# Kernel tuning notes

Measured on AMD Instinct MI355X. Metric: run time of the kernel, lower is better.

The kernel has to match this reference:

```python
import jax, jax.numpy as jnp
import numpy as np
import math

B, S, DM, H, F = 2, 2048, 1024, 16, 192  # F = head_dim init arg; per-head dim = F // 3
DH = F // 3
MAX_BIAS = 8.0


def _get_slopes(n):
    # faithful to ALiBiBias._get_slopes
    def pow2(n):
        start = 2.0 ** (-(2.0 ** (-(math.log2(n) - 3))))
        return [start * start ** i for i in range(n)]
    if math.log2(n).is_integer():
        return pow2(n)
    cp2 = 2 ** math.floor(math.log2(n))
    return pow2(cp2) + _get_slopes(2 * cp2)[0::2][: n - cp2]


def _rope_sin_cos(seq_len, dim):
    inv_freq = 1.0 / (10000.0 ** (jnp.arange(0, dim, 2, dtype=jnp.float32) / dim))
    freqs = jnp.outer(jnp.arange(seq_len, dtype=jnp.float32), inv_freq)  # [S, dim/2]
    # repeat(sin[:,None,:],2,axis=1).reshape(S,-1) == concat([sin,sin],-1)
    sin = jnp.concatenate([jnp.sin(freqs), jnp.sin(freqs)], axis=-1)  # [S, dim]
    cos = jnp.concatenate([jnp.cos(freqs), jnp.cos(freqs)], axis=-1)
    return sin, cos


def _rotate_half(x):
    x1, x2 = jnp.split(x, 2, axis=-1)
    return jnp.concatenate([-x2, x1], axis=-1)


def setup_inputs() -> dict:
    key = jax.random.key(0)
    kx, kq, ko = jax.random.split(key, 3)
    x = jax.random.normal(kx, (B, S, DM), dtype=jnp.float32)
    w_qkv = jax.random.normal(kq, (DM, H, F), dtype=jnp.float32) * (1.0 / math.sqrt(DM))
    b_qkv = jnp.zeros((H, F), dtype=jnp.float32)
    w_out = jax.random.normal(ko, (H, DH, DM), dtype=jnp.float32) * (1.0 / math.sqrt(H * DH))
    b_out = jnp.zeros((DM,), dtype=jnp.float32)
    return {"x": x, "w_qkv": w_qkv, "b_qkv": b_qkv, "w_out": w_out, "b_out": b_out}


def reference(x, w_qkv, b_qkv, w_out, b_out):
    b, s, dm = x.shape
    h, f = w_qkv.shape[1], w_qkv.shape[2]
    dh = f // 3
    # fused QKV projection: [B,S,H,F], then 3-way split on the feature axis
    qkv = jnp.einsum('bsd,dhf->bshf', x, w_qkv) + b_qkv
    q, k, v = jnp.split(qkv, 3, axis=-1)  # each [B,S,H,DH]
    # RoPE (rotate_half convention), broadcast over heads
    sin, cos = _rope_sin_cos(s, dh)
    sin, cos = sin[:, None, :], cos[:, None, :]  # [S,1,DH]
    q = q * cos + _rotate_half(q) * sin
    k = k * cos + _rotate_half(k) * sin
    # [B,H,S,DH]
    q = q.transpose(0, 2, 1, 3)
    k = k.transpose(0, 2, 1, 3)
    v = v.transpose(0, 2, 1, 3)
    # scores scaled by sqrt(head_dim init arg), as in the original non-flash path
    scores = jnp.einsum('bhqd,bhkd->bhqk', q, k) / jnp.sqrt(jnp.float32(f))
    # ALiBi bias
    slopes = jnp.asarray(_get_slopes(h), dtype=jnp.float32)  # [H]
    pos = jnp.arange(s, dtype=jnp.float32)
    rel = pos[None, :] - pos[:, None]  # j - i
    rel = jnp.where(rel > 0, 0.0, rel)
    alibi = rel[None, :, :] * slopes[:, None, None] * MAX_BIAS  # [H,S,S]
    scores = scores + alibi[None]  # [B,H,S,S]
    # causal mask
    causal = jnp.tril(jnp.ones((s, s), dtype=jnp.float32))
    scores = jnp.where(causal == 0, -1e9, scores)
    weights = jax.nn.softmax(scores, axis=-1)
    attn = jnp.einsum('bhqk,bhkd->bhqd', weights, v).transpose(0, 2, 1, 3)  # [B,S,H,DH]
    return jnp.einsum('bshd,hdm->bsm', attn, w_out) + b_out
```

## Files before the change

### kernel.cpp

```cpp
#include <hip/hip_runtime.h>
#include <math.h>

static constexpr int B_  = 2;
static constexpr int S_  = 2048;
static constexpr int H_  = 16;
static constexpr int DH_ = 64;
static constexpr float QSCALE2_ = 0.104117589f;
static constexpr float C8L2_    = 11.5415603f;

typedef __attribute__((ext_vector_type(8))) short short8;
typedef __attribute__((ext_vector_type(4))) float floatx4;

__device__ __forceinline__ float bf2f(unsigned short u) {
    union { unsigned int i; float f; } c; c.i = ((unsigned int)u) << 16; return c.f;
}
__device__ __forceinline__ unsigned short f2bf(float f) {
    union { float f; unsigned int i; } c; c.f = f;
    unsigned int x = c.i;
    unsigned int r = (x + 0x7fffu + ((x >> 16) & 1u)) >> 16;
    if ((x & 0x7f800000u) == 0x7f800000u) r = x >> 16;
    return (unsigned short)r;
}
__device__ __forceinline__ void load_lds16(const unsigned short* g, unsigned short* l) {
    __builtin_amdgcn_global_load_lds(
        (const __attribute__((address_space(1))) unsigned int*)g,
        (__attribute__((address_space(3))) unsigned int*)l, 16, 0, 0);
}

__global__ __launch_bounds__(256) void prep(
    const float* __restrict__ x,     unsigned short* __restrict__ xb,
    const float* __restrict__ w_qkv, unsigned short* __restrict__ wqkvT,
    const float* __restrict__ w_out, unsigned short* __restrict__ woutT)
{
    __shared__ float t[32][33];
    const int bid = blockIdx.x;
    if (bid < 4096) {
        const int i = bid * 256 + threadIdx.x;
        const float4 v = reinterpret_cast<const float4*>(x)[i];
        ushort4 r;
        r.x = f2bf(v.x); r.y = f2bf(v.y); r.z = f2bf(v.z); r.w = f2bf(v.w);
        reinterpret_cast<ushort4*>(xb)[i] = r;
        return;
    }
    const float* in; unsigned short* out; int NN, bx, by;
    if (bid < 7168) {
        in = w_qkv; out = wqkvT; NN = 3072;
        const int b2 = bid - 4096; bx = b2 % 96; by = b2 / 96;
    } else {
        in = w_out; out = woutT; NN = 1024;
        const int b2 = bid - 7168; bx = b2 & 31; by = b2 >> 5;
    }
    const int n0 = bx * 32;
    const int k0 = by * 32;
    const int tn = threadIdx.x & 31, tk = threadIdx.x >> 5;
    #pragma unroll
    for (int i = 0; i < 4; ++i)
        t[tk + 8 * i][tn] = in[(size_t)(k0 + tk + 8 * i) * NN + n0 + tn];
    __syncthreads();
    #pragma unroll
    for (int i = 0; i < 4; ++i)
        out[(size_t)(n0 + tk + 8 * i) * 1024 + k0 + tn] = f2bf(t[tn][tk + 8 * i]);
}

__global__ __launch_bounds__(256) void gemm_qkv(
    const unsigned short* __restrict__ A, const unsigned short* __restrict__ BT,
    const float* __restrict__ bias,
    unsigned short* __restrict__ O0, unsigned short* __restrict__ O1,
    unsigned short* __restrict__ O2)
{
    __shared__ unsigned short As[128 * 32];
    __shared__ unsigned short Bs[128 * 32];

    const int tid  = threadIdx.x;
    const int wave = tid >> 6;
    const int lane = tid & 63;
    const int quad = lane >> 4;
    const int lm   = lane & 15;
    const int wm = (wave >> 1) * 64;
    const int wn = (wave & 1) * 64;
    const int n0 = blockIdx.x * 128;
    const int m0 = blockIdx.y * 128;

    floatx4 acc[4][4] = {};

    const int sr = lane >> 2;
    const int sc = lane & 3;

    for (int k0 = 0; k0 < 1024; k0 += 32) {
        #pragma unroll
        for (int rep = 0; rep < 2; ++rep) {
            const int r = wave * 32 + rep * 16;
            load_lds16(A  + (size_t)(m0 + r + sr) * 1024 + k0 + sc * 8, &As[r * 32]);
            load_lds16(BT + (size_t)(n0 + r + sr) * 1024 + k0 + sc * 8, &Bs[r * 32]);
        }
        __syncthreads();
        short8 af[4], bf[4];
        #pragma unroll
        for (int i = 0; i < 4; ++i) {
            af[i] = *reinterpret_cast<const short8*>(&As[(wm + i * 16 + lm) * 32 + quad * 8]);
            bf[i] = *reinterpret_cast<const short8*>(&Bs[(wn + i * 16 + lm) * 32 + quad * 8]);
        }
        #pragma unroll
        for (int mi = 0; mi < 4; ++mi)
            #pragma unroll
            for (int ni = 0; ni < 4; ++ni)
                acc[mi][ni] = __builtin_amdgcn_mfma_f32_16x16x32_bf16(
                    af[mi], bf[ni], acc[mi][ni], 0, 0, 0);
        __syncthreads();
    }

    const int nbase = n0 + wn;
    const int h   = nbase / 192;
    const int sec = (nbase - h * 192) >> 6;
    float bia[4];
    #pragma unroll
    for (int ni = 0; ni < 4; ++ni) bia[ni] = bias[nbase + ni * 16 + lm];
    unsigned short* Out = (sec == 0) ? O0 : ((sec == 1) ? O1 : O2);

    if (sec == 2) {
        #pragma unroll
        for (int mi = 0; mi < 4; ++mi) {
            const int m  = m0 + wm + mi * 16 + quad * 4;
            const int bb = m >> 11;
            const int s  = m & (S_ - 1);
            const size_t rowb = (size_t)(bb * H_ + h) * DH_;
            #pragma unroll
            for (int ni = 0; ni < 4; ++ni) {
                const int d = ni * 16 + lm;
                ushort4 w;
                w.x = f2bf(acc[mi][ni][0] + bia[ni]);
                w.y = f2bf(acc[mi][ni][1] + bia[ni]);
                w.z = f2bf(acc[mi][ni][2] + bia[ni]);
                w.w = f2bf(acc[mi][ni][3] + bia[ni]);
                *reinterpret_cast<ushort4*>(&Out[(rowb + d) * S_ + s]) = w;
            }
        }
    } else {
        const float qscale = (sec == 0) ? QSCALE2_ : 1.0f;
        const float nlf = -13.287712379549449f / 32.0f;
        const float invf0 = exp2f((float)lm * nlf);
        const float invf1 = exp2f((float)(lm + 16) * nlf);
        #pragma unroll
        for (int mi = 0; mi < 4; ++mi) {
            #pragma unroll
            for (int r = 0; r < 4; ++r) {
                const int m  = m0 + wm + mi * 16 + quad * 4 + r;
                const int bb = m >> 11;
                const int s  = m & (S_ - 1);
                const size_t obase = ((size_t)(bb * H_ + h) * S_ + s) * DH_;
                const float a0 = (float)s * invf0, a1 = (float)s * invf1;
                const float sn0 = __sinf(a0), cs0 = __cosf(a0);
                const float sn1 = __sinf(a1), cs1 = __cosf(a1);
                #pragma unroll
                for (int ni = 0; ni < 4; ++ni) {
                    const int d = ni * 16 + lm;
                    const float v = acc[mi][ni][r]     + bia[ni];
                    const float p = acc[mi][ni ^ 2][r] + bia[ni ^ 2];
                    const float cs = (ni & 1) ? cs1 : cs0;
                    const float sn = (ni & 1) ? sn1 : sn0;
                    float res = (d < 32) ? (v * cs - p * sn) : (v * cs + p * sn);
                    Out[obase + d] = f2bf(res * qscale);
                }
            }
        }
    }
}

__global__ __launch_bounds__(256) void gemm_out(
    const unsigned short* __restrict__ A, const unsigned short* __restrict__ BT,
    const float* __restrict__ bias, float* __restrict__ Of)
{
    __shared__ unsigned short As[64 * 32];
    __shared__ unsigned short Bs[128 * 32];

    const int tid  = threadIdx.x;
    const int wave = tid >> 6;
    const int lane = tid & 63;
    const int quad = lane >> 4;
    const int lm   = lane & 15;
    const int wm = (wave >> 1) * 32;
    const int wn = (wave & 1) * 64;
    const int n0 = blockIdx.x * 128;
    const int m0 = blockIdx.y * 64;

    floatx4 acc[2][4] = {};

    const int sr = lane >> 2;
    const int sc = lane & 3;

    for (int k0 = 0; k0 < 1024; k0 += 32) {
        load_lds16(A + (size_t)(m0 + wave * 16 + sr) * 1024 + k0 + sc * 8,
                   &As[wave * 16 * 32]);
        #pragma unroll
        for (int rep = 0; rep < 2; ++rep) {
            const int r = wave * 32 + rep * 16;
            load_lds16(BT + (size_t)(n0 + r + sr) * 1024 + k0 + sc * 8, &Bs[r * 32]);
        }
        __syncthreads();
        short8 af[2], bf[4];
        #pragma unroll
        for (int i = 0; i < 2; ++i)
            af[i] = *reinterpret_cast<const short8*>(&As[(wm + i * 16 + lm) * 32 + quad * 8]);
        #pragma unroll
        for (int i = 0; i < 4; ++i)
            bf[i] = *reinterpret_cast<const short8*>(&Bs[(wn + i * 16 + lm) * 32 + quad * 8]);
        #pragma unroll
        for (int mi = 0; mi < 2; ++mi)
            #pragma unroll
            for (int ni = 0; ni < 4; ++ni)
                acc[mi][ni] = __builtin_amdgcn_mfma_f32_16x16x32_bf16(
                    af[mi], bf[ni], acc[mi][ni], 0, 0, 0);
        __syncthreads();
    }

    #pragma unroll
    for (int ni = 0; ni < 4; ++ni) {
        const int gn = n0 + wn + ni * 16 + lm;
        const float b = bias[gn];
        #pragma unroll
        for (int mi = 0; mi < 2; ++mi) {
            const int gm = m0 + wm + mi * 16 + quad * 4;
            #pragma unroll
            for (int r = 0; r < 4; ++r)
                Of[(size_t)(gm + r) * 1024 + gn] = acc[mi][ni][r] + b;
        }
    }
}

static constexpr int KST = 68;
static constexpr int PST = 68;

__global__ __launch_bounds__(256) void flash_mfma(
    const unsigned short* __restrict__ Q, const unsigned short* __restrict__ K,
    const unsigned short* __restrict__ VT, unsigned short* __restrict__ Ao)
{
    __shared__ unsigned short Ks[2][64 * KST];
    __shared__ unsigned short VTs[2][64 * KST];
    __shared__ unsigned short Ps[4][16 * PST];

    const int bi = blockIdx.x;
    const int bh = bi & 31;
    const int pr = bi >> 5;
    const int h  = bh & 15;
    const int b  = bh >> 4;
    const int tid  = threadIdx.x;
    const int wave = tid >> 6;
    const int lane = tid & 63;
    const int quad = lane >> 4;
    const int lm   = lane & 15;
    const int srow = tid >> 2;
    const int sc8  = tid & 3;

    const unsigned short* Kg  = K  + (size_t)bh * S_ * DH_;
    const unsigned short* VTg = VT + (size_t)bh * DH_ * S_;

    const float slope2 = exp2f(-0.5f * (float)(h + 1)) * (8.0f * 1.44269504f);
    const float d64 = 64.0f * slope2;

    int   koff[4];
    float alb[4];
    #pragma unroll
    for (int t = 0; t < 4; ++t) {
        koff[t] = t * 16 + quad * 4 - wave * 16 - lm;
        alb[t]  = (float)koff[t] * slope2 - C8L2_;
    }

    unsigned short* Pw = &Ps[wave][0];

    for (int ph = 0; ph < 2; ++ph) {
        const int qt = ph ? pr : 31 - pr;

        const unsigned short* Qrow =
            Q + ((size_t)bh * S_ + (size_t)(qt * 64 + wave * 16 + lm)) * DH_;
        const short8 aq0 = *reinterpret_cast<const short8*>(Qrow + quad * 8);
        const short8 aq1 = *reinterpret_cast<const short8*>(Qrow + 32 + quad * 8);

        float crk[4];
        #pragma unroll
        for (int r = 0; r < 4; ++r)
            crk[r] = (float)r * slope2 - (float)qt * d64;

        float l_one = 0.0f;
        floatx4 acc_o[4] = {};

        short8 ka, kb, va, vb;
        {
            const unsigned short* kr = Kg + (size_t)srow * DH_ + sc8 * 8;
            ka = *reinterpret_cast<const short8*>(kr);
            kb = *reinterpret_cast<const short8*>(kr + 32);
            const unsigned short* vr = VTg + (size_t)srow * S_ + sc8 * 8;
            va = *reinterpret_cast<const short8*>(vr);
            vb = *reinterpret_cast<const short8*>(vr + 32);
        }
        *reinterpret_cast<short8*>(&Ks[0][srow * KST + sc8 * 8])       = ka;
        *reinterpret_cast<short8*>(&Ks[0][srow * KST + sc8 * 8 + 32])  = kb;
        *reinterpret_cast<short8*>(&VTs[0][srow * KST + sc8 * 8])      = va;
        *reinterpret_cast<short8*>(&VTs[0][srow * KST + sc8 * 8 + 32]) = vb;
        if (qt > 0) {
            const unsigned short* kr = Kg + (size_t)(64 + srow) * DH_ + sc8 * 8;
            ka = *reinterpret_cast<const short8*>(kr);
            kb = *reinterpret_cast<const short8*>(kr + 32);
            const unsigned short* vr = VTg + (size_t)srow * S_ + 64 + sc8 * 8;
            va = *reinterpret_cast<const short8*>(vr);
            vb = *reinterpret_cast<const short8*>(vr + 32);
        }
        __syncthreads();

        for (int kt = 0; kt <= qt; ++kt) {
            const int cur = kt & 1;

            if (kt < qt) {
                const int nxt = cur ^ 1;
                *reinterpret_cast<short8*>(&Ks[nxt][srow * KST + sc8 * 8])       = ka;
                *reinterpret_cast<short8*>(&Ks[nxt][srow * KST + sc8 * 8 + 32])  = kb;
                *reinterpret_cast<short8*>(&VTs[nxt][srow * KST + sc8 * 8])      = va;
                *reinterpret_cast<short8*>(&VTs[nxt][srow * KST + sc8 * 8 + 32]) = vb;
                if (kt + 1 < qt) {
                    const unsigned short* kr =
                        Kg + (size_t)((kt + 2) * 64 + srow) * DH_ + sc8 * 8;
                    ka = *reinterpret_cast<const short8*>(kr);
                    kb = *reinterpret_cast<const short8*>(kr + 32);
                    const unsigned short* vr =
                        VTg + (size_t)srow * S_ + (kt + 2) * 64 + sc8 * 8;
                    va = *reinterpret_cast<const short8*>(vr);
                    vb = *reinterpret_cast<const short8*>(vr + 32);
                }
            }

            floatx4 sacc[4] = {};
            __builtin_amdgcn_s_setprio(1);
            #pragma unroll
            for (int t = 0; t < 4; ++t) {
                const short8 k0 = *reinterpret_cast<const short8*>(&Ks[cur][(t * 16 + lm) * KST + quad * 8]);
                const short8 k1 = *reinterpret_cast<const short8*>(&Ks[cur][(t * 16 + lm) * KST + 32 + quad * 8]);
                sacc[t] = __builtin_amdgcn_mfma_f32_16x16x32_bf16(k0, aq0, sacc[t], 0, 0, 0);
                sacc[t] = __builtin_amdgcn_mfma_f32_16x16x32_bf16(k1, aq1, sacc[t], 0, 0, 0);
            }
            __builtin_amdgcn_s_setprio(0);

            const bool diag = (kt == qt);
            #pragma unroll
            for (int t = 0; t < 4; ++t) {
                float p[4];
                #pragma unroll
                for (int r = 0; r < 4; ++r) {
                    const float x = (sacc[t][r] + alb[t]) + crk[r];
                    float e;
                    asm("v_exp_f32 %0, %1" : "=v"(e) : "v"(x));
                    if (diag && (koff[t] + r) > 0) e = 0.0f;
                    p[r] = e;
                }
                l_one += (p[0] + p[1]) + (p[2] + p[3]);
                unsigned int lo, hi;
                asm("v_cvt_pk_bf16_f32 %0, %1, %2" : "=v"(lo) : "v"(p[0]), "v"(p[1]));
                asm("v_cvt_pk_bf16_f32 %0, %1, %2" : "=v"(hi) : "v"(p[2]), "v"(p[3]));
                uint2 w; w.x = lo; w.y = hi;
                *reinterpret_cast<uint2*>(&Pw[lm * PST + t * 16 + quad * 4]) = w;
            }
            #pragma unroll
            for (int r = 0; r < 4; ++r) crk[r] += d64;

            const short8 ap0 = *reinterpret_cast<const short8*>(&Pw[lm * PST + quad * 8]);
            const short8 ap1 = *reinterpret_cast<const short8*>(&Pw[lm * PST + 32 + quad * 8]);
            __builtin_amdgcn_s_setprio(1);
            #pragma unroll
            for (int t = 0; t < 4; ++t) {
                const short8 v0 = *reinterpret_cast<const short8*>(&VTs[cur][(t * 16 + lm) * KST + quad * 8]);
                const short8 v1 = *reinterpret_cast<const short8*>(&VTs[cur][(t * 16 + lm) * KST + 32 + quad * 8]);
                acc_o[t] = __builtin_amdgcn_mfma_f32_16x16x32_bf16(ap0, v0, acc_o[t], 0, 0, 0);
                acc_o[t] = __builtin_amdgcn_mfma_f32_16x16x32_bf16(ap1, v1, acc_o[t], 0, 0, 0);
            }
            __builtin_amdgcn_s_setprio(0);
            __syncthreads();
        }

        l_one += __shfl_xor(l_one, 16);
        l_one += __shfl_xor(l_one, 32);
        #pragma unroll
        for (int r = 0; r < 4; ++r) {
            const float lr = __shfl(l_one, quad * 4 + r);
            const float inv_l = 1.0f / lr;
            const int s = qt * 64 + wave * 16 + quad * 4 + r;
            const size_t obase = ((size_t)(b * S_ + s) * H_ + h) * DH_;
            #pragma unroll
            for (int t = 0; t < 4; ++t)
                Ao[obase + t * 16 + lm] = f2bf(acc_o[t][r] * inv_l);
        }
    }
}

extern "C" void kernel_launch(void* const* d_in, const int* in_sizes, int n_in,
                              void* d_out, int out_size, void* d_ws, size_t ws_size,
                              hipStream_t stream)
{
    const float *x = nullptr, *w_qkv = nullptr, *b_qkv = nullptr,
                *w_out = nullptr, *b_out = nullptr;
    for (int i = 0; i < n_in; ++i) {
        switch (in_sizes[i]) {
            case 4194304: x     = (const float*)d_in[i]; break;
            case 3145728: w_qkv = (const float*)d_in[i]; break;
            case 3072:    b_qkv = (const float*)d_in[i]; break;
            case 1048576: w_out = (const float*)d_in[i]; break;
            case 1024:    b_out = (const float*)d_in[i]; break;
        }
    }
    if (!x)     x     = (const float*)d_in[0];
    if (!w_qkv) w_qkv = (const float*)d_in[1];
    if (!b_qkv) b_qkv = (const float*)d_in[2];
    if (!w_out) w_out = (const float*)d_in[3];
    if (!b_out) b_out = (const float*)d_in[4];

    float* out = (float*)d_out;
    unsigned short* ws16 = (unsigned short*)d_ws;

    unsigned short* xb     = ws16;
    unsigned short* wqkvT  = ws16 + (size_t)4194304;
    unsigned short* woutT  = ws16 + (size_t)7340032;
    unsigned short* Qb     = ws16 + (size_t)8388608;
    unsigned short* Kb     = ws16 + (size_t)12582912;
    unsigned short* Vb     = ws16 + (size_t)16777216;
    unsigned short* Aob    = ws16 + (size_t)20971520;

    prep<<<8192, 256, 0, stream>>>(x, xb, w_qkv, wqkvT, w_out, woutT);

    gemm_qkv<<<dim3(24, 32), 256, 0, stream>>>(
        xb, wqkvT, b_qkv, Qb, Kb, Vb);
    flash_mfma<<<dim3(512), 256, 0, stream>>>(Qb, Kb, Vb, Aob);
    gemm_out<<<dim3(8, 64), 256, 0, stream>>>(Aob, woutT, b_out, out);
}
```

Measured before the change: 192.9 us.

## Load K/V MFMA fragments directly from global into registers, drop LDS staging

Removes the shared-memory double buffer for K and V tiles. Each wave now loads its own MFMA operand fragments straight from global memory into registers and prefetches the next tile after each MFMA phase. This drops the per-iteration __syncthreads and the LDS write/read traffic, and launch_bounds now requests 2 blocks per CU. The cost is that each of the 4 waves reads the same K/V data from global/L2 separately, which is 4x the global load traffic, and the prefetch hides less latency than the two-ahead register pipeline it replaces.

```diff
diff --git a/kernel.cpp b/kernel.cpp
--- a/kernel.cpp
+++ b/kernel.cpp
@@ -227,15 +227,12 @@
     }
 }
 
-static constexpr int KST = 68;
 static constexpr int PST = 68;
 
-__global__ __launch_bounds__(256) void flash_mfma(
+__global__ __launch_bounds__(256, 2) void flash_mfma(
     const unsigned short* __restrict__ Q, const unsigned short* __restrict__ K,
     const unsigned short* __restrict__ VT, unsigned short* __restrict__ Ao)
 {
-    __shared__ unsigned short Ks[2][64 * KST];
-    __shared__ unsigned short VTs[2][64 * KST];
     __shared__ unsigned short Ps[4][16 * PST];
 
     const int bi = blockIdx.x;
@@ -248,11 +245,17 @@
     const int lane = tid & 63;
     const int quad = lane >> 4;
     const int lm   = lane & 15;
-    const int srow = tid >> 2;
-    const int sc8  = tid & 3;
 
     const unsigned short* Kg  = K  + (size_t)bh * S_ * DH_;
     const unsigned short* VTg = VT + (size_t)bh * DH_ * S_;
+
+    const unsigned short* kp[4];
+    const unsigned short* vp[4];
+    #pragma unroll
+    for (int t = 0; t < 4; ++t) {
+        kp[t] = Kg  + (size_t)(t * 16 + lm) * DH_ + quad * 8;
+        vp[t] = VTg + (size_t)(t * 16 + lm) * S_  + quad * 8;
+    }
 
     const float slope2 = exp2f(-0.5f * (float)(h + 1)) * (8.0f * 1.44269504f);
     const float d64 = 64.0f * slope2;
@@ -283,60 +286,33 @@
         float l_one = 0.0f;
         floatx4 acc_o[4] = {};
 
-        short8 ka, kb, va, vb;
-        {
-            const unsigned short* kr = Kg + (size_t)srow * DH_ + sc8 * 8;
-            ka = *reinterpret_cast<const short8*>(kr);
-            kb = *reinterpret_cast<const short8*>(kr + 32);
-            const unsigned short* vr = VTg + (size_t)srow * S_ + sc8 * 8;
-            va = *reinterpret_cast<const short8*>(vr);
-            vb = *reinterpret_cast<const short8*>(vr + 32);
-        }
-        *reinterpret_cast<short8*>(&Ks[0][srow * KST + sc8 * 8])       = ka;
-        *reinterpret_cast<short8*>(&Ks[0][srow * KST + sc8 * 8 + 32])  = kb;
-        *reinterpret_cast<short8*>(&VTs[0][srow * KST + sc8 * 8])      = va;
-        *reinterpret_cast<short8*>(&VTs[0][srow * KST + sc8 * 8 + 32]) = vb;
-        if (qt > 0) {
-            const unsigned short* kr = Kg + (size_t)(64 + srow) * DH_ + sc8 * 8;
-            ka = *reinterpret_cast<const short8*>(kr);
-            kb = *reinterpret_cast<const short8*>(kr + 32);
-            const unsigned short* vr = VTg + (size_t)srow * S_ + 64 + sc8 * 8;
-            va = *reinterpret_cast<const short8*>(vr);
-            vb = *reinterpret_cast<const short8*>(vr + 32);
-        }
-        __syncthreads();
+        short8 kf0[4], kf1[4], vf0[4], vf1[4];
+        #pragma unroll
+        for (int t = 0; t < 4; ++t) {
+            kf0[t] = *reinterpret_cast<const short8*>(kp[t]);
+            kf1[t] = *reinterpret_cast<const short8*>(kp[t] + 32);
+            vf0[t] = *reinterpret_cast<const short8*>(vp[t]);
+            vf1[t] = *reinterpret_cast<const short8*>(vp[t] + 32);
+        }
 
         for (int kt = 0; kt <= qt; ++kt) {
-            const int cur = kt & 1;
-
-            if (kt < qt) {
-                const int nxt = cur ^ 1;
-                *reinterpret_cast<short8*>(&Ks[nxt][srow * KST + sc8 * 8])       = ka;
-                *reinterpret_cast<short8*>(&Ks[nxt][srow * KST + sc8 * 8 + 32])  = kb;
-                *reinterpret_cast<short8*>(&VTs[nxt][srow * KST + sc8 * 8])      = va;
-                *reinterpret_cast<short8*>(&VTs[nxt][srow * KST + sc8 * 8 + 32]) = vb;
-                if (kt + 1 < qt) {
-                    const unsigned short* kr =
-                        Kg + (size_t)((kt + 2) * 64 + srow) * DH_ + sc8 * 8;
-                    ka = *reinterpret_cast<const short8*>(kr);
-                    kb = *reinterpret_cast<const short8*>(kr + 32);
-                    const unsigned short* vr =
-                        VTg + (size_t)srow * S_ + (kt + 2) * 64 + sc8 * 8;
-                    va = *reinterpret_cast<const short8*>(vr);
-                    vb = *reinterpret_cast<const short8*>(vr + 32);
-                }
-            }
-
             floatx4 sacc[4] = {};
             __builtin_amdgcn_s_setprio(1);
             #pragma unroll
             for (int t = 0; t < 4; ++t) {
-                const short8 k0 = *reinterpret_cast<const short8*>(&Ks[cur][(t * 16 + lm) * KST + quad * 8]);
-                const short8 k1 = *reinterpret_cast<const short8*>(&Ks[cur][(t * 16 + lm) * KST + 32 + quad * 8]);
-                sacc[t] = __builtin_amdgcn_mfma_f32_16x16x32_bf16(k0, aq0, sacc[t], 0, 0, 0);
-                sacc[t] = __builtin_amdgcn_mfma_f32_16x16x32_bf16(k1, aq1, sacc[t], 0, 0, 0);
+                sacc[t] = __builtin_amdgcn_mfma_f32_16x16x32_bf16(kf0[t], aq0, sacc[t], 0, 0, 0);
+                sacc[t] = __builtin_amdgcn_mfma_f32_16x16x32_bf16(kf1[t], aq1, sacc[t], 0, 0, 0);
             }
             __builtin_amdgcn_s_setprio(0);
+
+            if (kt < qt) {
+                const size_t off = (size_t)(kt + 1) * 64 * DH_;
+                #pragma unroll
+                for (int t = 0; t < 4; ++t) {
+                    kf0[t] = *reinterpret_cast<const short8*>(kp[t] + off);
+                    kf1[t] = *reinterpret_cast<const short8*>(kp[t] + off + 32);
+                }
+            }
 
             const bool diag = (kt == qt);
             #pragma unroll
@@ -365,13 +341,19 @@
             __builtin_amdgcn_s_setprio(1);
             #pragma unroll
             for (int t = 0; t < 4; ++t) {
-                const short8 v0 = *reinterpret_cast<const short8*>(&VTs[cur][(t * 16 + lm) * KST + quad * 8]);
-                const short8 v1 = *reinterpret_cast<const short8*>(&VTs[cur][(t * 16 + lm) * KST + 32 + quad * 8]);
-                acc_o[t] = __builtin_amdgcn_mfma_f32_16x16x32_bf16(ap0, v0, acc_o[t], 0, 0, 0);
-                acc_o[t] = __builtin_amdgcn_mfma_f32_16x16x32_bf16(ap1, v1, acc_o[t], 0, 0, 0);
+                acc_o[t] = __builtin_amdgcn_mfma_f32_16x16x32_bf16(ap0, vf0[t], acc_o[t], 0, 0, 0);
+                acc_o[t] = __builtin_amdgcn_mfma_f32_16x16x32_bf16(ap1, vf1[t], acc_o[t], 0, 0, 0);
             }
             __builtin_amdgcn_s_setprio(0);
-            __syncthreads();
+
+            if (kt < qt) {
+                const size_t off = (size_t)(kt + 1) * 64;
+                #pragma unroll
+                for (int t = 0; t < 4; ++t) {
+                    vf0[t] = *reinterpret_cast<const short8*>(vp[t] + off);
+                    vf1[t] = *reinterpret_cast<const short8*>(vp[t] + off + 32);
+                }
+            }
         }
 
         l_one += __shfl_xor(l_one, 16);
```

Measured after the change: 253.4 us. 1.31x slower.

## Process paired query tiles concurrently in 512-thread blocks sharing K/V tiles

Applied to the files above, without the earlier changes.

The flash kernel no longer handles its two paired query tiles (qt and 31-qt) one after the other. It now uses 8 waves per block: 4 waves handle the long tile and 4 the short tile, and both groups share each K/V tile loaded into shared memory. This drops the duplicate K/V loads for the short tile and lengthens the single loop, so there is more latency hiding per block. The cost is that the short-tile waves sit idle at barriers once their causal range is finished, and each block needs more LDS and registers.

```diff
diff --git a/kernel.cpp b/kernel.cpp
--- a/kernel.cpp
+++ b/kernel.cpp
@@ -230,17 +230,17 @@
 static constexpr int KST = 68;
 static constexpr int PST = 68;
 
-__global__ __launch_bounds__(256) void flash_mfma(
+__global__ __launch_bounds__(512, 4) void flash_mfma(
     const unsigned short* __restrict__ Q, const unsigned short* __restrict__ K,
     const unsigned short* __restrict__ VT, unsigned short* __restrict__ Ao)
 {
     __shared__ unsigned short Ks[2][64 * KST];
     __shared__ unsigned short VTs[2][64 * KST];
-    __shared__ unsigned short Ps[4][16 * PST];
+    __shared__ unsigned short Ps[8][16 * PST];
 
     const int bi = blockIdx.x;
     const int bh = bi & 31;
-    const int pr = bi >> 5;
+    const int p  = bi >> 5;
     const int h  = bh & 15;
     const int b  = bh >> 4;
     const int tid  = threadIdx.x;
@@ -248,8 +248,11 @@
     const int lane = tid & 63;
     const int quad = lane >> 4;
     const int lm   = lane & 15;
-    const int srow = tid >> 2;
-    const int sc8  = tid & 3;
+    const int wq   = wave & 3;
+    const int qt   = (wave < 4) ? (31 - p) : p;
+    const int nkt  = 32 - p;
+    const int srow = tid >> 3;
+    const int sc8  = tid & 7;
 
     const unsigned short* Kg  = K  + (size_t)bh * S_ * DH_;
     const unsigned short* VTg = VT + (size_t)bh * DH_ * S_;
@@ -261,72 +264,50 @@
     float alb[4];
     #pragma unroll
     for (int t = 0; t < 4; ++t) {
-        koff[t] = t * 16 + quad * 4 - wave * 16 - lm;
+        koff[t] = t * 16 + quad * 4 - wq * 16 - lm;
         alb[t]  = (float)koff[t] * slope2 - C8L2_;
     }
 
     unsigned short* Pw = &Ps[wave][0];
 
-    for (int ph = 0; ph < 2; ++ph) {
-        const int qt = ph ? pr : 31 - pr;
-
-        const unsigned short* Qrow =
-            Q + ((size_t)bh * S_ + (size_t)(qt * 64 + wave * 16 + lm)) * DH_;
-        const short8 aq0 = *reinterpret_cast<const short8*>(Qrow + quad * 8);
-        const short8 aq1 = *reinterpret_cast<const short8*>(Qrow + 32 + quad * 8);
-
-        float crk[4];
-        #pragma unroll
-        for (int r = 0; r < 4; ++r)
-            crk[r] = (float)r * slope2 - (float)qt * d64;
-
-        float l_one = 0.0f;
-        floatx4 acc_o[4] = {};
-
-        short8 ka, kb, va, vb;
-        {
-            const unsigned short* kr = Kg + (size_t)srow * DH_ + sc8 * 8;
-            ka = *reinterpret_cast<const short8*>(kr);
-            kb = *reinterpret_cast<const short8*>(kr + 32);
-            const unsigned short* vr = VTg + (size_t)srow * S_ + sc8 * 8;
-            va = *reinterpret_cast<const short8*>(vr);
-            vb = *reinterpret_cast<const short8*>(vr + 32);
-        }
-        *reinterpret_cast<short8*>(&Ks[0][srow * KST + sc8 * 8])       = ka;
-        *reinterpret_cast<short8*>(&Ks[0][srow * KST + sc8 * 8 + 32])  = kb;
-        *reinterpret_cast<short8*>(&VTs[0][srow * KST + sc8 * 8])      = va;
-        *reinterpret_cast<short8*>(&VTs[0][srow * KST + sc8 * 8 + 32]) = vb;
-        if (qt > 0) {
-            const unsigned short* kr = Kg + (size_t)(64 + srow) * DH_ + sc8 * 8;
-            ka = *reinterpret_cast<const short8*>(kr);
-            kb = *reinterpret_cast<const short8*>(kr + 32);
-            const unsigned short* vr = VTg + (size_t)srow * S_ + 64 + sc8 * 8;
-            va = *reinterpret_cast<const short8*>(vr);
-            vb = *reinterpret_cast<const short8*>(vr + 32);
-        }
-        __syncthreads();
-
-        for (int kt = 0; kt <= qt; ++kt) {
-            const int cur = kt & 1;
-
-            if (kt < qt) {
-                const int nxt = cur ^ 1;
-                *reinterpret_cast<short8*>(&Ks[nxt][srow * KST + sc8 * 8])       = ka;
-                *reinterpret_cast<short8*>(&Ks[nxt][srow * KST + sc8 * 8 + 32])  = kb;
-                *reinterpret_cast<short8*>(&VTs[nxt][srow * KST + sc8 * 8])      = va;
-                *reinterpret_cast<short8*>(&VTs[nxt][srow * KST + sc8 * 8 + 32]) = vb;
-                if (kt + 1 < qt) {
-                    const unsigned short* kr =
-                        Kg + (size_t)((kt + 2) * 64 + srow) * DH_ + sc8 * 8;
-                    ka = *reinterpret_cast<const short8*>(kr);
-                    kb = *reinterpret_cast<const short8*>(kr + 32);
-                    const unsigned short* vr =
-                        VTg + (size_t)srow * S_ + (kt + 2) * 64 + sc8 * 8;
-                    va = *reinterpret_cast<const short8*>(vr);
-                    vb = *reinterpret_cast<const short8*>(vr + 32);
-                }
-            }
-
+    const unsigned short* Qrow =
+        Q + ((size_t)bh * S_ + (size_t)(qt * 64 + wq * 16 + lm)) * DH_;
+    const short8 aq0 = *reinterpret_cast<const short8*>(Qrow + quad * 8);
+    const short8 aq1 = *reinterpret_cast<const short8*>(Qrow + 32 + quad * 8);
+
+    float crk[4];
+    #pragma unroll
+    for (int r = 0; r < 4; ++r)
+        crk[r] = (float)r * slope2 - (float)qt * d64;
+
+    float l_one = 0.0f;
+    floatx4 acc_o[4] = {};
+
+    short8 ka, va;
+    ka = *reinterpret_cast<const short8*>(Kg + (size_t)srow * DH_ + sc8 * 8);
+    va = *reinterpret_cast<const short8*>(VTg + (size_t)srow * S_ + sc8 * 8);
+    *reinterpret_cast<short8*>(&Ks[0][srow * KST + sc8 * 8])  = ka;
+    *reinterpret_cast<short8*>(&VTs[0][srow * KST + sc8 * 8]) = va;
+    ka = *reinterpret_cast<const short8*>(Kg + (size_t)(64 + srow) * DH_ + sc8 * 8);
+    va = *reinterpret_cast<const short8*>(VTg + (size_t)srow * S_ + 64 + sc8 * 8);
+    __syncthreads();
+
+    for (int kt = 0; kt < nkt; ++kt) {
+        const int cur = kt & 1;
+
+        if (kt + 1 < nkt) {
+            const int nxt = cur ^ 1;
+            *reinterpret_cast<short8*>(&Ks[nxt][srow * KST + sc8 * 8])  = ka;
+            *reinterpret_cast<short8*>(&VTs[nxt][srow * KST + sc8 * 8]) = va;
+            if (kt + 2 < nkt) {
+                ka = *reinterpret_cast<const short8*>(
+                    Kg + (size_t)((kt + 2) * 64 + srow) * DH_ + sc8 * 8);
+                va = *reinterpret_cast<const short8*>(
+                    VTg + (size_t)srow * S_ + (kt + 2) * 64 + sc8 * 8);
+            }
+        }
+
+        if (kt <= qt) {
             floatx4 sacc[4] = {};
             __builtin_amdgcn_s_setprio(1);
             #pragma unroll
@@ -341,19 +322,19 @@
             const bool diag = (kt == qt);
             #pragma unroll
             for (int t = 0; t < 4; ++t) {
-                float p[4];
+                float pv[4];
                 #pragma unroll
                 for (int r = 0; r < 4; ++r) {
                     const float x = (sacc[t][r] + alb[t]) + crk[r];
                     float e;
                     asm("v_exp_f32 %0, %1" : "=v"(e) : "v"(x));
                     if (diag && (koff[t] + r) > 0) e = 0.0f;
-                    p[r] = e;
+                    pv[r] = e;
                 }
-                l_one += (p[0] + p[1]) + (p[2] + p[3]);
+                l_one += (pv[0] + pv[1]) + (pv[2] + pv[3]);
                 unsigned int lo, hi;
-                asm("v_cvt_pk_bf16_f32 %0, %1, %2" : "=v"(lo) : "v"(p[0]), "v"(p[1]));
-                asm("v_cvt_pk_bf16_f32 %0, %1, %2" : "=v"(hi) : "v"(p[2]), "v"(p[3]));
+                asm("v_cvt_pk_bf16_f32 %0, %1, %2" : "=v"(lo) : "v"(pv[0]), "v"(pv[1]));
+                asm("v_cvt_pk_bf16_f32 %0, %1, %2" : "=v"(hi) : "v"(pv[2]), "v"(pv[3]));
                 uint2 w; w.x = lo; w.y = hi;
                 *reinterpret_cast<uint2*>(&Pw[lm * PST + t * 16 + quad * 4]) = w;
             }
@@ -371,21 +352,21 @@
                 acc_o[t] = __builtin_amdgcn_mfma_f32_16x16x32_bf16(ap1, v1, acc_o[t], 0, 0, 0);
             }
             __builtin_amdgcn_s_setprio(0);
-            __syncthreads();
-        }
-
-        l_one += __shfl_xor(l_one, 16);
-        l_one += __shfl_xor(l_one, 32);
-        #pragma unroll
-        for (int r = 0; r < 4; ++r) {
-            const float lr = __shfl(l_one, quad * 4 + r);
-            const float inv_l = 1.0f / lr;
-            const int s = qt * 64 + wave * 16 + quad * 4 + r;
-            const size_t obase = ((size_t)(b * S_ + s) * H_ + h) * DH_;
-            #pragma unroll
-            for (int t = 0; t < 4; ++t)
-                Ao[obase + t * 16 + lm] = f2bf(acc_o[t][r] * inv_l);
-        }
+        }
+        __syncthreads();
+    }
+
+    l_one += __shfl_xor(l_one, 16);
+    l_one += __shfl_xor(l_one, 32);
+    #pragma unroll
+    for (int r = 0; r < 4; ++r) {
+        const float lr = __shfl(l_one, quad * 4 + r);
+        const float inv_l = 1.0f / lr;
+        const int s = qt * 64 + wq * 16 + quad * 4 + r;
+        const size_t obase = ((size_t)(b * S_ + s) * H_ + h) * DH_;
+        #pragma unroll
+        for (int t = 0; t < 4; ++t)
+            Ao[obase + t * 16 + lm] = f2bf(acc_o[t][r] * inv_l);
     }
 }
 
@@ -425,6 +406,6 @@
 
     gemm_qkv<<<dim3(24, 32), 256, 0, stream>>>(
         xb, wqkvT, b_qkv, Qb, Kb, Vb);
-    flash_mfma<<<dim3(512), 256, 0, stream>>>(Qb, Kb, Vb, Aob);
+    flash_mfma<<<dim3(512), 512, 0, stream>>>(Qb, Kb, Vb, Aob);
     gemm_out<<<dim3(8, 64), 256, 0, stream>>>(Aob, woutT, b_out, out);
 }
```

After: 186.9 us. -3.1%, faster.

## Swizzle flash LDS tiles and launch one query tile per block

Applied to the files above, without the earlier changes.

Replaces the padded LDS rows (stride 68) with unpadded 64-wide rows and an XOR swizzle on the 16-byte chunk index, used for the K, V^T and P tiles, so reads avoid bank conflicts with less shared memory. It also removes the paired-tile loop: each block now handles one query tile, with heavy tiles scheduled first, and the grid doubles to 1024 blocks. A launch-bounds occupancy hint of 4 is added. The trade is that causal load balancing now relies on the hardware block scheduler instead of explicit pairing, and Q loads and the prologue are repeated per block.

```diff
diff --git a/kernel.cpp b/kernel.cpp
--- a/kernel.cpp
+++ b/kernel.cpp
@@ -227,20 +227,17 @@
     }
 }
 
-static constexpr int KST = 68;
-static constexpr int PST = 68;
-
-__global__ __launch_bounds__(256) void flash_mfma(
+__global__ __launch_bounds__(256, 4) void flash_mfma(
     const unsigned short* __restrict__ Q, const unsigned short* __restrict__ K,
     const unsigned short* __restrict__ VT, unsigned short* __restrict__ Ao)
 {
-    __shared__ unsigned short Ks[2][64 * KST];
-    __shared__ unsigned short VTs[2][64 * KST];
-    __shared__ unsigned short Ps[4][16 * PST];
+    __shared__ unsigned short Ks[2][64 * 64];
+    __shared__ unsigned short VTs[2][64 * 64];
+    __shared__ unsigned short Ps[4][16 * 64];
 
     const int bi = blockIdx.x;
+    const int qt = 31 - (bi >> 5);
     const int bh = bi & 31;
-    const int pr = bi >> 5;
     const int h  = bh & 15;
     const int b  = bh >> 4;
     const int tid  = threadIdx.x;
@@ -251,6 +248,11 @@
     const int srow = tid >> 2;
     const int sc8  = tid & 3;
 
+    const int swa = (sc8)     ^ (srow & 7);
+    const int swb = (sc8 + 4) ^ (srow & 7);
+    const int rq0 = (quad)     ^ (lm & 7);
+    const int rq1 = (quad + 4) ^ (lm & 7);
+
     const unsigned short* Kg  = K  + (size_t)bh * S_ * DH_;
     const unsigned short* VTg = VT + (size_t)bh * DH_ * S_;
 
@@ -266,126 +268,126 @@
     }
 
     unsigned short* Pw = &Ps[wave][0];
-
-    for (int ph = 0; ph < 2; ++ph) {
-        const int qt = ph ? pr : 31 - pr;
-
-        const unsigned short* Qrow =
-            Q + ((size_t)bh * S_ + (size_t)(qt * 64 + wave * 16 + lm)) * DH_;
-        const short8 aq0 = *reinterpret_cast<const short8*>(Qrow + quad * 8);
-        const short8 aq1 = *reinterpret_cast<const short8*>(Qrow + 32 + quad * 8);
-
-        float crk[4];
-        #pragma unroll
-        for (int r = 0; r < 4; ++r)
-            crk[r] = (float)r * slope2 - (float)qt * d64;
-
-        float l_one = 0.0f;
-        floatx4 acc_o[4] = {};
-
-        short8 ka, kb, va, vb;
-        {
-            const unsigned short* kr = Kg + (size_t)srow * DH_ + sc8 * 8;
-            ka = *reinterpret_cast<const short8*>(kr);
-            kb = *reinterpret_cast<const short8*>(kr + 32);
-            const unsigned short* vr = VTg + (size_t)srow * S_ + sc8 * 8;
-            va = *reinterpret_cast<const short8*>(vr);
-            vb = *reinterpret_cast<const short8*>(vr + 32);
-        }
-        *reinterpret_cast<short8*>(&Ks[0][srow * KST + sc8 * 8])       = ka;
-        *reinterpret_cast<short8*>(&Ks[0][srow * KST + sc8 * 8 + 32])  = kb;
-        *reinterpret_cast<short8*>(&VTs[0][srow * KST + sc8 * 8])      = va;
-        *reinterpret_cast<short8*>(&VTs[0][srow * KST + sc8 * 8 + 32]) = vb;
-        if (qt > 0) {
-            const unsigned short* kr = Kg + (size_t)(64 + srow) * DH_ + sc8 * 8;
-            ka = *reinterpret_cast<const short8*>(kr);
-            kb = *reinterpret_cast<const short8*>(kr + 32);
-            const unsigned short* vr = VTg + (size_t)srow * S_ + 64 + sc8 * 8;
-            va = *reinterpret_cast<const short8*>(vr);
-            vb = *reinterpret_cast<const short8*>(vr + 32);
-        }
+    int pwr[4];
+    #pragma unroll
+    for (int t = 0; t < 4; ++t)
+        pwr[t] = lm * 64 + ((2 * t + (quad >> 1)) ^ (lm & 7)) * 8 + (quad & 1) * 4;
+
+    const unsigned short* Qrow =
+        Q + ((size_t)bh * S_ + (size_t)(qt * 64 + wave * 16 + lm)) * DH_;
+    const short8 aq0 = *reinterpret_cast<const short8*>(Qrow + quad * 8);
+    const short8 aq1 = *reinterpret_cast<const short8*>(Qrow + 32 + quad * 8);
+
+    float crk[4];
+    #pragma unroll
+    for (int r = 0; r < 4; ++r)
+        crk[r] = (float)r * slope2 - (float)qt * d64;
+
+    float l_one = 0.0f;
+    floatx4 acc_o[4] = {};
+
+    short8 ka, kb, va, vb;
+    {
+        const unsigned short* kr = Kg + (size_t)srow * DH_ + sc8 * 8;
+        ka = *reinterpret_cast<const short8*>(kr);
+        kb = *reinterpret_cast<const short8*>(kr + 32);
+        const unsigned short* vr = VTg + (size_t)srow * S_ + sc8 * 8;
+        va = *reinterpret_cast<const short8*>(vr);
+        vb = *reinterpret_cast<const short8*>(vr + 32);
+    }
+    *reinterpret_cast<short8*>(&Ks[0][srow * 64 + swa * 8])  = ka;
+    *reinterpret_cast<short8*>(&Ks[0][srow * 64 + swb * 8])  = kb;
+    *reinterpret_cast<short8*>(&VTs[0][srow * 64 + swa * 8]) = va;
+    *reinterpret_cast<short8*>(&VTs[0][srow * 64 + swb * 8]) = vb;
+    if (qt > 0) {
+        const unsigned short* kr = Kg + (size_t)(64 + srow) * DH_ + sc8 * 8;
+        ka = *reinterpret_cast<const short8*>(kr);
+        kb = *reinterpret_cast<const short8*>(kr + 32);
+        const unsigned short* vr = VTg + (size_t)srow * S_ + 64 + sc8 * 8;
+        va = *reinterpret_cast<const short8*>(vr);
+        vb = *reinterpret_cast<const short8*>(vr + 32);
+    }
+    __syncthreads();
+
+    for (int kt = 0; kt <= qt; ++kt) {
+        const int cur = kt & 1;
+
+        if (kt < qt) {
+            const int nxt = cur ^ 1;
+            *reinterpret_cast<short8*>(&Ks[nxt][srow * 64 + swa * 8])  = ka;
+            *reinterpret_cast<short8*>(&Ks[nxt][srow * 64 + swb * 8])  = kb;
+            *reinterpret_cast<short8*>(&VTs[nxt][srow * 64 + swa * 8]) = va;
+            *reinterpret_cast<short8*>(&VTs[nxt][srow * 64 + swb * 8]) = vb;
+            if (kt + 1 < qt) {
+                const unsigned short* kr =
+                    Kg + (size_t)((kt + 2) * 64 + srow) * DH_ + sc8 * 8;
+                ka = *reinterpret_cast<const short8*>(kr);
+                kb = *reinterpret_cast<const short8*>(kr + 32);
+                const unsigned short* vr =
+                    VTg + (size_t)srow * S_ + (kt + 2) * 64 + sc8 * 8;
+                va = *reinterpret_cast<const short8*>(vr);
+                vb = *reinterpret_cast<const short8*>(vr + 32);
+            }
+        }
+
+        floatx4 sacc[4] = {};
+        __builtin_amdgcn_s_setprio(1);
+        #pragma unroll
+        for (int t = 0; t < 4; ++t) {
+            const short8 k0 = *reinterpret_cast<const short8*>(&Ks[cur][(t * 16 + lm) * 64 + rq0 * 8]);
+            const short8 k1 = *reinterpret_cast<const short8*>(&Ks[cur][(t * 16 + lm) * 64 + rq1 * 8]);
+            sacc[t] = __builtin_amdgcn_mfma_f32_16x16x32_bf16(k0, aq0, sacc[t], 0, 0, 0);
+            sacc[t] = __builtin_amdgcn_mfma_f32_16x16x32_bf16(k1, aq1, sacc[t], 0, 0, 0);
+        }
+        __builtin_amdgcn_s_setprio(0);
+
+        const bool diag = (kt == qt);
+        #pragma unroll
+        for (int t = 0; t < 4; ++t) {
+            float pv[4];
+            #pragma unroll
+            for (int r = 0; r < 4; ++r) {
+                const float x = (sacc[t][r] + alb[t]) + crk[r];
+                float e;
+                asm("v_exp_f32 %0, %1" : "=v"(e) : "v"(x));
+                if (diag && (koff[t] + r) > 0) e = 0.0f;
+                pv[r] = e;
+            }
+            l_one += (pv[0] + pv[1]) + (pv[2] + pv[3]);
+            unsigned int lo, hi;
+            asm("v_cvt_pk_bf16_f32 %0, %1, %2" : "=v"(lo) : "v"(pv[0]), "v"(pv[1]));
+            asm("v_cvt_pk_bf16_f32 %0, %1, %2" : "=v"(hi) : "v"(pv[2]), "v"(pv[3]));
+            uint2 w; w.x = lo; w.y = hi;
+            *reinterpret_cast<uint2*>(&Pw[pwr[t]]) = w;
+        }
+        #pragma unroll
+        for (int r = 0; r < 4; ++r) crk[r] += d64;
+
+        const short8 ap0 = *reinterpret_cast<const short8*>(&Pw[lm * 64 + rq0 * 8]);
+        const short8 ap1 = *reinterpret_cast<const short8*>(&Pw[lm * 64 + rq1 * 8]);
+        __builtin_amdgcn_s_setprio(1);
+        #pragma unroll
+        for (int t = 0; t < 4; ++t) {
+            const short8 v0 = *reinterpret_cast<const short8*>(&VTs[cur][(t * 16 + lm) * 64 + rq0 * 8]);
+            const short8 v1 = *reinterpret_cast<const short8*>(&VTs[cur][(t * 16 + lm) * 64 + rq1 * 8]);
+            acc_o[t] = __builtin_amdgcn_mfma_f32_16x16x32_bf16(ap0, v0, acc_o[t], 0, 0, 0);
+            acc_o[t] = __builtin_amdgcn_mfma_f32_16x16x32_bf16(ap1, v1, acc_o[t], 0, 0, 0);
+        }
+        __builtin_amdgcn_s_setprio(0);
         __syncthreads();
-
-        for (int kt = 0; kt <= qt; ++kt) {
-            const int cur = kt & 1;
-
-            if (kt < qt) {
-                const int nxt = cur ^ 1;
-                *reinterpret_cast<short8*>(&Ks[nxt][srow * KST + sc8 * 8])       = ka;
-                *reinterpret_cast<short8*>(&Ks[nxt][srow * KST + sc8 * 8 + 32])  = kb;
-                *reinterpret_cast<short8*>(&VTs[nxt][srow * KST + sc8 * 8])      = va;
-                *reinterpret_cast<short8*>(&VTs[nxt][srow * KST + sc8 * 8 + 32]) = vb;
-                if (kt + 1 < qt) {
-                    const unsigned short* kr =
-                        Kg + (size_t)((kt + 2) * 64 + srow) * DH_ + sc8 * 8;
-                    ka = *reinterpret_cast<const short8*>(kr);
-                    kb = *reinterpret_cast<const short8*>(kr + 32);
-                    const unsigned short* vr =
-                        VTg + (size_t)srow * S_ + (kt + 2) * 64 + sc8 * 8;
-                    va = *reinterpret_cast<const short8*>(vr);
-                    vb = *reinterpret_cast<const short8*>(vr + 32);
-                }
-            }
-
-            floatx4 sacc[4] = {};
-            __builtin_amdgcn_s_setprio(1);
-            #pragma unroll
-            for (int t = 0; t < 4; ++t) {
-                const short8 k0 = *reinterpret_cast<const short8*>(&Ks[cur][(t * 16 + lm) * KST + quad * 8]);
-                const short8 k1 = *reinterpret_cast<const short8*>(&Ks[cur][(t * 16 + lm) * KST + 32 + quad * 8]);
-                sacc[t] = __builtin_amdgcn_mfma_f32_16x16x32_bf16(k0, aq0, sacc[t], 0, 0, 0);
-                sacc[t] = __builtin_amdgcn_mfma_f32_16x16x32_bf16(k1, aq1, sacc[t], 0, 0, 0);
-            }
-            __builtin_amdgcn_s_setprio(0);
-
-            const bool diag = (kt == qt);
-            #pragma unroll
-            for (int t = 0; t < 4; ++t) {
-                float p[4];
-                #pragma unroll
-                for (int r = 0; r < 4; ++r) {
-                    const float x = (sacc[t][r] + alb[t]) + crk[r];
-                    float e;
-                    asm("v_exp_f32 %0, %1" : "=v"(e) : "v"(x));
-                    if (diag && (koff[t] + r) > 0) e = 0.0f;
-                    p[r] = e;
-                }
-                l_one += (p[0] + p[1]) + (p[2] + p[3]);
-                unsigned int lo, hi;
-                asm("v_cvt_pk_bf16_f32 %0, %1, %2" : "=v"(lo) : "v"(p[0]), "v"(p[1]));
-                asm("v_cvt_pk_bf16_f32 %0, %1, %2" : "=v"(hi) : "v"(p[2]), "v"(p[3]));
-                uint2 w; w.x = lo; w.y = hi;
-                *reinterpret_cast<uint2*>(&Pw[lm * PST + t * 16 + quad * 4]) = w;
-            }
-            #pragma unroll
-            for (int r = 0; r < 4; ++r) crk[r] += d64;
-
-            const short8 ap0 = *reinterpret_cast<const short8*>(&Pw[lm * PST + quad * 8]);
-            const short8 ap1 = *reinterpret_cast<const short8*>(&Pw[lm * PST + 32 + quad * 8]);
-            __builtin_amdgcn_s_setprio(1);
-            #pragma unroll
-            for (int t = 0; t < 4; ++t) {
-                const short8 v0 = *reinterpret_cast<const short8*>(&VTs[cur][(t * 16 + lm) * KST + quad * 8]);
-                const short8 v1 = *reinterpret_cast<const short8*>(&VTs[cur][(t * 16 + lm) * KST + 32 + quad * 8]);
-                acc_o[t] = __builtin_amdgcn_mfma_f32_16x16x32_bf16(ap0, v0, acc_o[t], 0, 0, 0);
-                acc_o[t] = __builtin_amdgcn_mfma_f32_16x16x32_bf16(ap1, v1, acc_o[t], 0, 0, 0);
-            }
-            __builtin_amdgcn_s_setprio(0);
-            __syncthreads();
-        }
-
-        l_one += __shfl_xor(l_one, 16);
-        l_one += __shfl_xor(l_one, 32);
-        #pragma unroll
-        for (int r = 0; r < 4; ++r) {
-            const float lr = __shfl(l_one, quad * 4 + r);
-            const float inv_l = 1.0f / lr;
-            const int s = qt * 64 + wave * 16 + quad * 4 + r;
-            const size_t obase = ((size_t)(b * S_ + s) * H_ + h) * DH_;
-            #pragma unroll
-            for (int t = 0; t < 4; ++t)
-                Ao[obase + t * 16 + lm] = f2bf(acc_o[t][r] * inv_l);
-        }
+    }
+
+    l_one += __shfl_xor(l_one, 16);
+    l_one += __shfl_xor(l_one, 32);
+    #pragma unroll
+    for (int r = 0; r < 4; ++r) {
+        const float lr = __shfl(l_one, quad * 4 + r);
+        const float inv_l = 1.0f / lr;
+        const int s = qt * 64 + wave * 16 + quad * 4 + r;
+        const size_t obase = ((size_t)(b * S_ + s) * H_ + h) * DH_;
+        #pragma unroll
+        for (int t = 0; t < 4; ++t)
+            Ao[obase + t * 16 + lm] = f2bf(acc_o[t][r] * inv_l);
     }
 }
 
@@ -425,6 +427,6 @@
 
     gemm_qkv<<<dim3(24, 32), 256, 0, stream>>>(
         xb, wqkvT, b_qkv, Qb, Kb, Vb);
-    flash_mfma<<<dim3(512), 256, 0, stream>>>(Qb, Kb, Vb, Aob);
+    flash_mfma<<<dim3(1024), 256, 0, stream>>>(Qb, Kb, Vb, Aob);
     gemm_out<<<dim3(8, 64), 256, 0, stream>>>(Aob, woutT, b_out, out);
 }
```

New measurement: 174.7 us. -9.5%, faster.
